# Optimization experiments

Measured on AMD Instinct MI355X. Metric: run time of the kernel, lower is better.

## Reference

```python
import jax, jax.numpy as jnp
import numpy as np

WINDOW = 11
PAD = WINDOW // 2
C1 = 0.01 ** 2
C2 = 0.03 ** 2


def _avg_pool(x):
    # Matches torch F.avg_pool2d(x, k, stride=1, padding=k//2) with
    # count_include_pad=True (default): sum over zero-padded window / k^2.
    # Separable box filter: sum over H then W.
    s = jax.lax.reduce_window(
        x, 0.0, jax.lax.add,
        window_dimensions=(1, 1, WINDOW, 1), window_strides=(1, 1, 1, 1),
        padding=((0, 0), (0, 0), (PAD, PAD), (0, 0)))
    s = jax.lax.reduce_window(
        s, 0.0, jax.lax.add,
        window_dimensions=(1, 1, 1, WINDOW), window_strides=(1, 1, 1, 1),
        padding=((0, 0), (0, 0), (0, 0), (PAD, PAD)))
    return s * (1.0 / (WINDOW * WINDOW))


def setup_inputs() -> dict:
    key = jax.random.key(0)
    k1, k2 = jax.random.split(key)
    shape = (16, 3, 512, 512)
    pred = jax.random.uniform(k1, shape, dtype=jnp.float32)
    target = jax.random.uniform(k2, shape, dtype=jnp.float32)
    return {"pred": pred, "target": target}


def reference(pred, target):
    mu_x = _avg_pool(pred)
    mu_y = _avg_pool(target)
    mu_x_sq = mu_x * mu_x
    mu_y_sq = mu_y * mu_y
    mu_xy = mu_x * mu_y
    sigma_x = _avg_pool(pred * pred) - mu_x_sq
    sigma_y = _avg_pool(target * target) - mu_y_sq
    sigma_xy = _avg_pool(pred * target) - mu_xy
    ssim_map = ((2.0 * mu_xy + C1) * (2.0 * sigma_xy + C2)
                / ((mu_x_sq + mu_y_sq + C1) * (sigma_x + sigma_y + C2)))
    ssim_map = jnp.clip(ssim_map, 0.0, 1.0)
    # per-sample loss: 1 - mean over C,H,W
    return 1.0 - jnp.mean(ssim_map.reshape(ssim_map.shape[0], -1), axis=1)
```

## Files before the change

kernel.cpp:

```cpp
#include <hip/hip_runtime.h>

#define HH 512
#define WW 512
#define NCH 3
#define NBATCH 16
#define NIMG (NBATCH*NCH)
#define CHUNK 16
#define NCHUNK (HH/CHUNK)
#define NSTRIP 4
#define SW 128
#define SLOTS 142
#define NWAVE 4
#define NT (64*NWAVE)
#define NUNITS (NIMG*NCHUNK*NSTRIP)
#define BLKS_PER_B (NCH*NCHUNK*NSTRIP)

struct RowData { float4 m; float2 h; };

__global__ __launch_bounds__(NT) void ssim_main(
    const float* __restrict__ pred, const float* __restrict__ targ,
    float* __restrict__ ws)
{
  __shared__ __align__(16) float2 arrA[NWAVE][SLOTS];
  __shared__ __align__(16) float2 arrB[NWAVE][SLOTS];

  const int tid = threadIdx.x;
  const int wid = tid >> 6;
  const int l   = tid & 63;
  const int unit = blockIdx.x * NWAVE + wid;
  const int img = unit >> 7;
  const int rem = unit & 127;
  const int chunk = rem >> 2;
  const int strip = rem & 3;

  const int r0 = chunk*CHUNK - 5;
  const int c0 = strip*SW;

  const size_t ib = (size_t)img * (size_t)(HH*WW);
  const float* pp = pred + ib;
  const float* tp = targ + ib;

  const int cm = c0 + 2*l;
  const int h  = l - 54;
  const int ch = (h < 5) ? (c0 - 5 + h) : (c0 + 123 + h);
  const bool hval = (l >= 54) && ((unsigned)ch < (unsigned)WW);
  const int chc = min(max(ch, 0), WW-1);
  const int hs = (h < 5) ? (1 + h) : (129 + h);

  float2* const wA = arrA[wid];
  float2* const wB = arrB[wid];

  auto loadrow_nb = [&](int it) -> RowData {
    const int r = r0 + it;
    const int rc = min(max(r, 0), HH-1);
    const float mask = ((unsigned)r < (unsigned)HH) ? 1.f : 0.f;
    const float hm = hval ? mask : 0.f;
    const size_t ro = (size_t)rc * WW;
    const float2 x = *(const float2*)(pp + ro + cm);
    const float2 y = *(const float2*)(tp + ro + cm);
    const float hx = pp[ro + chc], hy = tp[ro + chc];
    RowData d;
    d.m = make_float4(x.x*mask, x.y*mask, y.x*mask, y.y*mask);
    d.h = make_float2(hx*hm, hy*hm);
    return d;
  };

  float vx0=0.f, vy0=0.f, vxy0=0.f, vss0=0.f;
  float vx1=0.f, vy1=0.f, vxy1=0.f, vss1=0.f;
  float vxh=0.f, vyh=0.f, vxyh=0.f, vssh=0.f;
  float acc = 0.f;

  const RowData zrow = { make_float4(0.f,0.f,0.f,0.f), make_float2(0.f,0.f) };

  RowData curN = loadrow_nb(0);
  RowData nxtN = loadrow_nb(1);
  RowData nx2N = loadrow_nb(2);

  constexpr float c1 = 0.0001f, c2 = 0.0009f, inv121 = 1.0f/121.0f;

  auto ssim1 = [&](float Sx, float Sy, float Sxy, float Sss) -> float {
    const float mux = Sx*inv121, muy = Sy*inv121;
    const float muxy = mux*muy;
    const float m2   = fmaf(mux, mux, muy*muy);
    const float sgxy = fmaf(Sxy, inv121, -muxy);
    const float sgss = fmaf(Sss, inv121, -m2);
    const float num = fmaf(2.f, muxy, c1) * fmaf(2.f, sgxy, c2);
    const float den = (m2 + c1) * (sgss + c2);
    const float s = num * __builtin_amdgcn_rcpf(den);
    return fminf(fmaxf(s, 0.f), 1.f);
  };

  auto slide = [&](const RowData& nw, const RowData& od) {
    const float xn0 = nw.m.x, xn1 = nw.m.y;
    const float yn0 = nw.m.z, yn1 = nw.m.w;
    const float xo0 = od.m.x, xo1 = od.m.y;
    const float yo0 = od.m.z, yo1 = od.m.w;
    vx0  += xn0 - xo0;  vy0  += yn0 - yo0;
    vx1  += xn1 - xo1;  vy1  += yn1 - yo1;
    vxy0 += xn0*yn0 - xo0*yo0;
    vxy1 += xn1*yn1 - xo1*yo1;
    vss0 += fmaf(xn0, xn0, yn0*yn0) - fmaf(xo0, xo0, yo0*yo0);
    vss1 += fmaf(xn1, xn1, yn1*yn1) - fmaf(xo1, xo1, yo1*yo1);
    const float xnh = nw.h.x, ynh = nw.h.y;
    const float xoh = od.h.x, yoh = od.h.y;
    vxh  += xnh - xoh;  vyh  += ynh - yoh;
    vxyh += xnh*ynh - xoh*yoh;
    vssh += fmaf(xnh, xnh, ynh*ynh) - fmaf(xoh, xoh, yoh*yoh);
  };

  auto advN = [&](int it) {
    curN = nxtN; nxtN = nx2N;
    nx2N = loadrow_nb(it + 3);
  };

  #pragma clang loop unroll_count(2)
  for (int it = 0; it < 8; ++it) {
    slide(curN, zrow);
    advN(it);
  }
  slide(curN, zrow); advN(8);
  RowData o1 = loadrow_nb(0);
  slide(curN, zrow); advN(9);
  RowData o2 = loadrow_nb(1);
  RowData o0 = zrow;

  #pragma clang loop unroll_count(2)
  for (int it = 10; it < 26; ++it) {
    slide(curN, o0);

    advN(it);
    o0 = o1; o1 = o2;
    o2 = loadrow_nb(it - 8);

    *(float4*)(wA + 6 + 2*l) = make_float4(vx0, vy0, vx1, vy1);
    *(float4*)(wB + 6 + 2*l) = make_float4(vxy0, vss0, vxy1, vss1);
    if (l >= 54) {
      wA[hs] = make_float2(vxh, vyh);
      wB[hs] = make_float2(vxyh, vssh);
    }

    const float4* ta = (const float4*)(wA) + l;
    const float4 a0v = ta[0], a1v = ta[1], a2v = ta[2], a3v = ta[3],
                 a4v = ta[4], a5v = ta[5], a6v = ta[6];
    const float4* tb = (const float4*)(wB) + l;
    const float4 b0v = tb[0], b1v = tb[1], b2v = tb[2], b3v = tb[3],
                 b4v = tb[4], b5v = tb[5], b6v = tb[6];

    float Sx = a0v.z, Sy = a0v.w;
    Sx += a1v.x; Sy += a1v.y;  Sx += a1v.z; Sy += a1v.w;
    Sx += a2v.x; Sy += a2v.y;  Sx += a2v.z; Sy += a2v.w;
    Sx += a3v.x; Sy += a3v.y;  Sx += a3v.z; Sy += a3v.w;
    Sx += a4v.x; Sy += a4v.y;  Sx += a4v.z; Sy += a4v.w;
    Sx += a5v.x; Sy += a5v.y;  Sx += a5v.z; Sy += a5v.w;
    const float Sx1 = Sx - a0v.z + a6v.x;
    const float Sy1 = Sy - a0v.w + a6v.y;

    float Sxy = b0v.z, Sss = b0v.w;
    Sxy += b1v.x; Sss += b1v.y;  Sxy += b1v.z; Sss += b1v.w;
    Sxy += b2v.x; Sss += b2v.y;  Sxy += b2v.z; Sss += b2v.w;
    Sxy += b3v.x; Sss += b3v.y;  Sxy += b3v.z; Sss += b3v.w;
    Sxy += b4v.x; Sss += b4v.y;  Sxy += b4v.z; Sss += b4v.w;
    Sxy += b5v.x; Sss += b5v.y;  Sxy += b5v.z; Sss += b5v.w;
    const float Sxy1 = Sxy - b0v.z + b6v.x;
    const float Sss1 = Sss - b0v.w + b6v.y;

    acc += ssim1(Sx,  Sy,  Sxy,  Sss);
    acc += ssim1(Sx1, Sy1, Sxy1, Sss1);
  }

  #pragma unroll
  for (int off = 32; off > 0; off >>= 1) acc += __shfl_down(acc, off, 64);
  if (l == 0) ws[unit] = acc;
}

__global__ void ssim_final(const float* __restrict__ ws, float* __restrict__ out) {
  const int b = blockIdx.x;
  const int t = threadIdx.x;
  const float* p = ws + b * BLKS_PER_B;
  float s = 0.f;
  #pragma unroll
  for (int k = 0; k < BLKS_PER_B/64; ++k) s += p[t + 64*k];
  #pragma unroll
  for (int off = 32; off > 0; off >>= 1) s += __shfl_down(s, off, 64);
  if (t == 0) out[b] = 1.0f - s * (1.0f / (float)(NCH*HH*WW));
}

extern "C" void kernel_launch(void* const* d_in, const int* in_sizes, int n_in,
                              void* d_out, int out_size, void* d_ws, size_t ws_size,
                              hipStream_t stream) {
  const float* pred = (const float*)d_in[0];
  const float* targ = (const float*)d_in[1];
  float* out = (float*)d_out;
  float* ws  = (float*)d_ws;
  ssim_main<<<dim3(NUNITS/NWAVE), dim3(NT), 0, stream>>>(pred, targ, ws);
  ssim_final<<<dim3(NBATCH), dim3(64), 0, stream>>>(ws, out);
}
```

Baseline: 141.5 us.

## Replace LDS horizontal box sum with wave shuffles over overlapping strips

```diff
diff --git a/kernel.cpp b/kernel.cpp
--- a/kernel.cpp
+++ b/kernel.cpp
@@ -7,74 +7,60 @@
 #define NIMG (NBATCH*NCH)
 #define CHUNK 16
 #define NCHUNK (HH/CHUNK)
-#define NSTRIP 4
-#define SW 128
-#define SLOTS 142
+#define NSTRIP 5
 #define NWAVE 4
 #define NT (64*NWAVE)
 #define NUNITS (NIMG*NCHUNK*NSTRIP)
 #define BLKS_PER_B (NCH*NCHUNK*NSTRIP)
 
-struct RowData { float4 m; float2 h; };
-
 __global__ __launch_bounds__(NT) void ssim_main(
     const float* __restrict__ pred, const float* __restrict__ targ,
     float* __restrict__ ws)
 {
-  __shared__ __align__(16) float2 arrA[NWAVE][SLOTS];
-  __shared__ __align__(16) float2 arrB[NWAVE][SLOTS];
-
   const int tid = threadIdx.x;
   const int wid = tid >> 6;
   const int l   = tid & 63;
   const int unit = blockIdx.x * NWAVE + wid;
-  const int img = unit >> 7;
-  const int rem = unit & 127;
-  const int chunk = rem >> 2;
-  const int strip = rem & 3;
+  const int img = unit / (NCHUNK*NSTRIP);
+  const int rem = unit % (NCHUNK*NSTRIP);
+  const int chunk = rem / NSTRIP;
+  const int strip = rem % NSTRIP;
 
   const int r0 = chunk*CHUNK - 5;
-  const int c0 = strip*SW;
+  const int e0 = strip * 104;
+  const int sw = (strip == 4) ? 96 : 104;
+  const int lhi = 3 + (sw >> 1);
 
   const size_t ib = (size_t)img * (size_t)(HH*WW);
   const float* pp = pred + ib;
   const float* tp = targ + ib;
 
-  const int cm = c0 + 2*l;
-  const int h  = l - 54;
-  const int ch = (h < 5) ? (c0 - 5 + h) : (c0 + 123 + h);
-  const bool hval = (l >= 54) && ((unsigned)ch < (unsigned)WW);
-  const int chc = min(max(ch, 0), WW-1);
-  const int hs = (h < 5) ? (1 + h) : (129 + h);
+  const int cl0 = e0 - 6 + 2*l;
+  const int cl1 = cl0 + 1;
+  const int cl0c = min(max(cl0, 0), WW-2);
+  const float colm0 = ((unsigned)cl0 < (unsigned)WW) ? 1.f : 0.f;
+  const float colm1 = ((unsigned)cl1 < (unsigned)WW) ? 1.f : 0.f;
 
-  float2* const wA = arrA[wid];
-  float2* const wB = arrB[wid];
-
-  auto loadrow_nb = [&](int it) -> RowData {
+  auto loadrow_nb = [&](int it) -> float4 {
     const int r = r0 + it;
     const int rc = min(max(r, 0), HH-1);
-    const float mask = ((unsigned)r < (unsigned)HH) ? 1.f : 0.f;
-    const float hm = hval ? mask : 0.f;
-    const size_t ro = (size_t)rc * WW;
-    const float2 x = *(const float2*)(pp + ro + cm);
-    const float2 y = *(const float2*)(tp + ro + cm);
-    const float hx = pp[ro + chc], hy = tp[ro + chc];
-    RowData d;
-    d.m = make_float4(x.x*mask, x.y*mask, y.x*mask, y.y*mask);
-    d.h = make_float2(hx*hm, hy*hm);
-    return d;
+    const float rowm = ((unsigned)r < (unsigned)HH) ? 1.f : 0.f;
+    const float m0 = colm0 * rowm, m1 = colm1 * rowm;
+    const size_t ro = (size_t)rc * WW + cl0c;
+    const float2 x = *(const float2*)(pp + ro);
+    const float2 y = *(const float2*)(tp + ro);
+    return make_float4(x.x*m0, x.y*m1, y.x*m0, y.y*m1);
   };
 
-  float vx0=0.f, vy0=0.f, vxy0=0.f, vss0=0.f;
-  float vx1=0.f, vy1=0.f, vxy1=0.f, vss1=0.f;
-  float vxh=0.f, vyh=0.f, vxyh=0.f, vssh=0.f;
+  float vx0=0.f, vx1=0.f, vy0=0.f, vy1=0.f;
+  float vxy0=0.f, vxy1=0.f, vss0=0.f, vss1=0.f;
   float acc = 0.f;
 
-  const RowData zrow = { make_float4(0.f,0.f,0.f,0.f), make_float2(0.f,0.f) };
+  const float4 z4 = make_float4(0.f, 0.f, 0.f, 0.f);
 
-  RowData curN = loadrow_nb(0);
-  RowData nxtN = loadrow_nb(1);
-  RowData nx2N = loadrow_nb(2);
+  float4 curN = loadrow_nb(0);
+  float4 nxtN = loadrow_nb(1);
+  float4 nx2N = loadrow_nb(2);
 
   constexpr float c1 = 0.0001f, c2 = 0.0009f, inv121 = 1.0f/121.0f;
 
@@ -90,22 +76,13 @@
     return fminf(fmaxf(s, 0.f), 1.f);
   };
 
-  auto slide = [&](const RowData& nw, const RowData& od) {
-    const float xn0 = nw.m.x, xn1 = nw.m.y;
-    const float yn0 = nw.m.z, yn1 = nw.m.w;
-    const float xo0 = od.m.x, xo1 = od.m.y;
-    const float yo0 = od.m.z, yo1 = od.m.w;
-    vx0  += xn0 - xo0;  vy0  += yn0 - yo0;
-    vx1  += xn1 - xo1;  vy1  += yn1 - yo1;
-    vxy0 += xn0*yn0 - xo0*yo0;
-    vxy1 += xn1*yn1 - xo1*yo1;
-    vss0 += fmaf(xn0, xn0, yn0*yn0) - fmaf(xo0, xo0, yo0*yo0);
-    vss1 += fmaf(xn1, xn1, yn1*yn1) - fmaf(xo1, xo1, yo1*yo1);
-    const float xnh = nw.h.x, ynh = nw.h.y;
-    const float xoh = od.h.x, yoh = od.h.y;
-    vxh  += xnh - xoh;  vyh  += ynh - yoh;
-    vxyh += xnh*ynh - xoh*yoh;
-    vssh += fmaf(xnh, xnh, ynh*ynh) - fmaf(xoh, xoh, yoh*yoh);
+  auto slide = [&](const float4 n, const float4 o) {
+    vx0  += n.x - o.x;        vx1  += n.y - o.y;
+    vy0  += n.z - o.z;        vy1  += n.w - o.w;
+    vxy0 += n.x*n.z - o.x*o.z;
+    vxy1 += n.y*n.w - o.y*o.w;
+    vss0 += fmaf(n.x, n.x, n.z*n.z) - fmaf(o.x, o.x, o.z*o.z);
+    vss1 += fmaf(n.y, n.y, n.w*n.w) - fmaf(o.y, o.y, o.w*o.w);
   };
 
   auto advN = [&](int it) {
@@ -113,59 +90,47 @@
     nx2N = loadrow_nb(it + 3);
   };
 
+  auto win = [&](float E, float O, float& W0, float& W1) {
+    const float Q = E + O;
+    float T = Q;
+    T += __shfl(Q, l - 1, 64);
+    T += __shfl(Q, l + 1, 64);
+    T += __shfl(Q, l - 2, 64);
+    T += __shfl(Q, l + 2, 64);
+    W0 = __shfl(O, l - 3, 64) + T;
+    W1 = T + __shfl(E, l + 3, 64);
+  };
+
+  auto emit = [&]() {
+    float W0x, W1x, W0y, W1y, W0xy, W1xy, W0ss, W1ss;
+    win(vx0,  vx1,  W0x,  W1x);
+    win(vy0,  vy1,  W0y,  W1y);
+    win(vxy0, vxy1, W0xy, W1xy);
+    win(vss0, vss1, W0ss, W1ss);
+    if (l >= 3 && l < lhi) {
+      acc += ssim1(W0x, W0y, W0xy, W0ss);
+      acc += ssim1(W1x, W1y, W1xy, W1ss);
+    }
+  };
+
   #pragma clang loop unroll_count(2)
   for (int it = 0; it < 8; ++it) {
-    slide(curN, zrow);
+    slide(curN, z4);
     advN(it);
   }
-  slide(curN, zrow); advN(8);
-  RowData o1 = loadrow_nb(0);
-  slide(curN, zrow); advN(9);
-  RowData o2 = loadrow_nb(1);
-  RowData o0 = zrow;
+  slide(curN, z4); advN(8);
+  float4 o1 = loadrow_nb(0);
+  slide(curN, z4); advN(9);
+  float4 o2 = loadrow_nb(1);
+  float4 o0 = z4;
 
   #pragma clang loop unroll_count(2)
   for (int it = 10; it < 26; ++it) {
     slide(curN, o0);
-
     advN(it);
     o0 = o1; o1 = o2;
     o2 = loadrow_nb(it - 8);
-
-    *(float4*)(wA + 6 + 2*l) = make_float4(vx0, vy0, vx1, vy1);
-    *(float4*)(wB + 6 + 2*l) = make_float4(vxy0, vss0, vxy1, vss1);
-    if (l >= 54) {
-      wA[hs] = make_float2(vxh, vyh);
-      wB[hs] = make_float2(vxyh, vssh);
-    }
-
-    const float4* ta = (const float4*)(wA) + l;
-    const float4 a0v = ta[0], a1v = ta[1], a2v = ta[2], a3v = ta[3],
-                 a4v = ta[4], a5v = ta[5], a6v = ta[6];
-    const float4* tb = (const float4*)(wB) + l;
-    const float4 b0v = tb[0], b1v = tb[1], b2v = tb[2], b3v = tb[3],
-                 b4v = tb[4], b5v = tb[5], b6v = tb[6];
-
-    float Sx = a0v.z, Sy = a0v.w;
-    Sx += a1v.x; Sy += a1v.y;  Sx += a1v.z; Sy += a1v.w;
-    Sx += a2v.x; Sy += a2v.y;  Sx += a2v.z; Sy += a2v.w;
-    Sx += a3v.x; Sy += a3v.y;  Sx += a3v.z; Sy += a3v.w;
-    Sx += a4v.x; Sy += a4v.y;  Sx += a4v.z; Sy += a4v.w;
-    Sx += a5v.x; Sy += a5v.y;  Sx += a5v.z; Sy += a5v.w;
-    const float Sx1 = Sx - a0v.z + a6v.x;
-    const float Sy1 = Sy - a0v.w + a6v.y;
-
-    float Sxy = b0v.z, Sss = b0v.w;
-    Sxy += b1v.x; Sss += b1v.y;  Sxy += b1v.z; Sss += b1v.w;
-    Sxy += b2v.x; Sss += b2v.y;  Sxy += b2v.z; Sss += b2v.w;
-    Sxy += b3v.x; Sss += b3v.y;  Sxy += b3v.z; Sss += b3v.w;
-    Sxy += b4v.x; Sss += b4v.y;  Sxy += b4v.z; Sss += b4v.w;
-    Sxy += b5v.x; Sss += b5v.y;  Sxy += b5v.z; Sss += b5v.w;
-    const float Sxy1 = Sxy - b0v.z + b6v.x;
-    const float Sss1 = Sss - b0v.w + b6v.y;
-
-    acc += ssim1(Sx,  Sy,  Sxy,  Sss);
-    acc += ssim1(Sx1, Sy1, Sxy1, Sss1);
+    emit();
   }
 
   #pragma unroll
@@ -179,7 +144,8 @@
   const float* p = ws + b * BLKS_PER_B;
   float s = 0.f;
   #pragma unroll
-  for (int k = 0; k < BLKS_PER_B/64; ++k) s += p[t + 64*k];
+  for (int k = 0; k < 7; ++k) s += p[t + 64*k];
+  if (t < 32) s += p[t + 448];
   #pragma unroll
   for (int off = 32; off > 0; off >>= 1) s += __shfl_down(s, off, 64);
   if (t == 0) out[b] = 1.0f - s * (1.0f / (float)(NCH*HH*WW));
```

Result: no change. 141.1 us (-0.3%).
